# Kernel optimization log

Measured on AMD Instinct MI355X. Metric: run time of the kernel, lower is better.

The kernel has to match this reference:

```python
import jax, jax.numpy as jnp
import numpy as np

N_NODES = 100000


def gcn_conv(x, edge_index, edge_weight, W, b, num_nodes):
    """PyG-style GCNConv: add self-loops, symmetric normalization, aggregate, linear."""
    src, dst = edge_index[0], edge_index[1]
    loop = jnp.arange(num_nodes, dtype=src.dtype)
    src_f = jnp.concatenate([src, loop])
    dst_f = jnp.concatenate([dst, loop])
    w_f = jnp.concatenate([edge_weight, jnp.ones((num_nodes,), dtype=edge_weight.dtype)])

    # symmetric normalization D^-1/2 A_hat D^-1/2
    deg = jax.ops.segment_sum(w_f, dst_f, num_segments=num_nodes)
    dinv = jnp.where(deg > 0, jax.lax.rsqrt(deg), 0.0)
    norm = dinv[src_f] * w_f * dinv[dst_f]  # [E + N]

    h = x @ W  # transform first (small out dim) -> cheaper gather/scatter
    msg = h[src_f] * norm[:, None]  # [E + N, out]
    out = jax.ops.segment_sum(msg, dst_f, num_segments=num_nodes)
    return out + b


def setup_inputs() -> dict:
    key = jax.random.key(0)
    k = jax.random.split(key, 7)
    N, E, F, H, C = N_NODES, 3200000, 64, 32, 5
    x = jax.random.normal(k[0], (N, F), dtype=jnp.float32)
    edge_index = jax.random.randint(k[1], (2, E), 0, N, dtype=jnp.int64)
    edge_attr = jax.random.uniform(k[2], (E,), dtype=jnp.float32)
    # Glorot-style init for GCNConv weights, zero bias (PyG default)
    W1 = jax.random.normal(k[3], (F, H), dtype=jnp.float32) * (1.0 / np.sqrt(F))
    b1 = jnp.zeros((H,), dtype=jnp.float32)
    W2 = jax.random.normal(k[4], (H, C), dtype=jnp.float32) * (1.0 / np.sqrt(H))
    b2 = jnp.zeros((C,), dtype=jnp.float32)
    return {"x": x, "edge_index": edge_index, "edge_attr": edge_attr,
            "W1": W1, "b1": b1, "W2": W2, "b2": b2}


def reference(x, edge_index, edge_attr, W1, b1, W2, b2):
    # Dropout is identity in eval mode.
    x1 = gcn_conv(x, edge_index, edge_attr, W1, b1, N_NODES)
    x1 = jax.nn.relu(x1)
    x2 = gcn_conv(x1, edge_index, edge_attr, W2, b2, N_NODES)
    return (x2, x1)
```

## Files before the change

kernel.cpp:

```cpp
#include <hip/hip_runtime.h>

#define NN 100000
#define NE 3200000
#define FIN 64
#define FH 32
#define FO 5
#define NB 1000
#define NPB 100
#define NBIN (4*NPB)
#define QDIV 25000
#define GC 512
#define EPB (NE/GC)
#define KPT 25
#define APAD 6252
#define DPAD 6272
#define CAP 3584
#define WQS 32767.f
#define WQI (1.0f/32767.f)

typedef unsigned u32x4 __attribute__((ext_vector_type(4)));

__device__ __forceinline__ int detect64(const int* __restrict__ ei, int* sflag, int tid) {
    if (tid < 64) {
        int v = ei[2 * tid + 1];
        unsigned long long m = __ballot(v == 0);
        if (tid == 0) *sflag = (m == ~0ULL) ? 1 : 0;
    }
    __syncthreads();
    return *sflag;
}

__device__ __forceinline__ unsigned bf16r(float f) {
    unsigned u = __float_as_uint(f);
    return (u + 0x7FFFu + ((u >> 16) & 1u)) >> 16;
}
__device__ __forceinline__ float blo(unsigned u) { return __uint_as_float(u << 16); }
__device__ __forceinline__ float bhi(unsigned u) { return __uint_as_float(u & 0xFFFF0000u); }

__global__ void k_fillC(const int* __restrict__ ei, const float* __restrict__ w,
                        int* __restrict__ cntRM, int* __restrict__ locRM,
                        unsigned* __restrict__ edata_a, unsigned char* __restrict__ edata_d) {
    __shared__ unsigned stage_a[EPB];
    __shared__ unsigned char stage_d[EPB];
    __shared__ int hist[NB];
    __shared__ int hoff[NB];
    __shared__ int sscan[256];
    __shared__ int sflag;
    int tid = threadIdx.x, g = blockIdx.x;
    for (int i = tid; i < NB; i += 256) hist[i] = 0;
    int is64 = detect64(ei, &sflag, tid);
    __syncthreads();
    int base = g * EPB;
    int myd[KPT];
#pragma unroll
    for (int k = 0; k < KPT; ++k) {
        int e = base + tid + k * 256;
        int dst = -1;
        if (e < base + EPB) {
            dst = is64 ? ei[2 * NE + 2 * e] : ei[NE + e];
            atomicAdd(&hist[dst / NPB], 1);
        }
        myd[k] = dst;
    }
    __syncthreads();
    for (int i = tid; i < NB; i += 256) cntRM[g * NB + i] = hist[i];
    int b0 = tid * 4;
    int c0 = (b0 + 0 < NB) ? hist[b0 + 0] : 0;
    int c1 = (b0 + 1 < NB) ? hist[b0 + 1] : 0;
    int c2 = (b0 + 2 < NB) ? hist[b0 + 2] : 0;
    int c3 = (b0 + 3 < NB) ? hist[b0 + 3] : 0;
    sscan[tid] = c0 + c1 + c2 + c3;
    __syncthreads();
    for (int off = 1; off < 256; off <<= 1) {
        int v = (tid >= off) ? sscan[tid - off] : 0;
        __syncthreads();
        sscan[tid] += v;
        __syncthreads();
    }
    int excl = sscan[tid] - (c0 + c1 + c2 + c3);
    if (b0 + 0 < NB) { hoff[b0 + 0] = excl;                locRM[g * NB + b0 + 0] = excl; }
    if (b0 + 1 < NB) { hoff[b0 + 1] = excl + c0;           locRM[g * NB + b0 + 1] = excl + c0; }
    if (b0 + 2 < NB) { hoff[b0 + 2] = excl + c0 + c1;      locRM[g * NB + b0 + 2] = excl + c0 + c1; }
    if (b0 + 3 < NB) { hoff[b0 + 3] = excl + c0 + c1 + c2; locRM[g * NB + b0 + 3] = excl + c0 + c1 + c2; }
    __syncthreads();
#pragma unroll
    for (int k = 0; k < KPT; ++k) {
        int e = base + tid + k * 256;
        if (e < base + EPB) {
            int src = is64 ? ei[2 * e] : ei[e];
            int dst = myd[k];
            int b = dst / NPB;
            int dloc = dst - b * NPB;
            unsigned wq = (unsigned)(w[e] * WQS + 0.5f);
            int pos = atomicAdd(&hoff[b], 1);
            stage_a[pos] = (unsigned)src | (wq << 17);
            stage_d[pos] = (unsigned char)dloc;
        }
    }
    __syncthreads();
    unsigned* ga = edata_a + (size_t)g * APAD;
    int4* ga4 = (int4*)ga;
    const int NI4 = EPB / 4;
    for (int i = tid; i < NI4; i += 256) {
        int4 v;
        v.x = (int)stage_a[4 * i];     v.y = (int)stage_a[4 * i + 1];
        v.z = (int)stage_a[4 * i + 2]; v.w = (int)stage_a[4 * i + 3];
        ga4[i] = v;
    }
    if (tid < EPB - NI4 * 4) ga[NI4 * 4 + tid] = stage_a[NI4 * 4 + tid];
    unsigned* gd = (unsigned*)(edata_d + (size_t)g * DPAD);
    const int ND = (EPB + 3) / 4;
    for (int i = tid; i < ND; i += 256) {
        unsigned b0v = stage_d[4 * i];
        unsigned b1v = (4 * i + 1 < EPB) ? stage_d[4 * i + 1] : 0;
        unsigned b2v = (4 * i + 2 < EPB) ? stage_d[4 * i + 2] : 0;
        unsigned b3v = (4 * i + 3 < EPB) ? stage_d[4 * i + 3] : 0;
        gd[i] = b0v | (b1v << 8) | (b2v << 16) | (b3v << 24);
    }
}

__global__ __launch_bounds__(512) void k_nodecsr(
        const int* __restrict__ cntRM, const int* __restrict__ locRM,
        const unsigned* __restrict__ edata_a, const unsigned char* __restrict__ edata_d,
        unsigned* __restrict__ edata2,
        int* __restrict__ rowS, int* __restrict__ rowE, float* __restrict__ dinv) {
    __shared__ unsigned s1a[CAP];
    __shared__ unsigned char s1d[CAP];
    __shared__ unsigned s2a[CAP];
    __shared__ int cnt[NBIN];
    __shared__ int loc[NBIN];
    __shared__ int sc[512];
    __shared__ int llocS[512];
    __shared__ int sBlen;
    int* cur = cnt;
    int* degS = (int*)s2a;
    int bi = blockIdx.x, tid = threadIdx.x;
    int b = (bi & 7) * (NB / 8) + (bi >> 3);
    int base = b * CAP;
    int g = tid;
    int len  = cntRM[g * NB + b];
    int lloc = locRM[g * NB + b];
    llocS[tid] = lloc;
    for (int i = tid; i < NBIN; i += 512) cnt[i] = 0;
    if (tid < NPB) degS[tid] = 0;
    sc[tid] = len;
    __syncthreads();
    for (int off = 1; off < 512; off <<= 1) {
        int x = (tid >= off) ? sc[tid - off] : 0;
        __syncthreads();
        sc[tid] += x;
        __syncthreads();
    }
    if (tid == 511) sBlen = sc[511];
    __syncthreads();
    int blen = sBlen;
    if (blen <= CAP) {
        for (int j = tid; j < blen; j += 512) {
            int g2 = 0;
#pragma unroll
            for (int st = 256; st > 0; st >>= 1)
                if (g2 + st < 512 && sc[g2 + st - 1] <= j) g2 += st;
            int sd = g2 ? sc[g2 - 1] : 0;
            int off = j - sd;
            int ll = llocS[g2];
            unsigned a = edata_a[(size_t)g2 * APAD + ll + off];
            int dloc = edata_d[(size_t)g2 * DPAD + ll + off];
            int src = (int)(a & 0x1FFFF);
            atomicAdd(&cnt[(dloc << 2) | (src / QDIV)], 1);
            atomicAdd(&degS[dloc], (int)(a >> 17));
            s1a[j] = a;
            s1d[j] = (unsigned char)dloc;
        }
        __syncthreads();
        int v = (tid < NBIN) ? cnt[tid] : 0;
        sc[tid] = v;
        __syncthreads();
        for (int off = 1; off < 512; off <<= 1) {
            int x = (tid >= off) ? sc[tid - off] : 0;
            __syncthreads();
            sc[tid] += x;
            __syncthreads();
        }
        if (tid < NBIN) { loc[tid] = sc[tid] - v; }
        __syncthreads();
        if (tid < NBIN) cur[tid] = loc[tid];
        if (tid < NPB) {
            rowS[b * NPB + tid] = base + loc[4 * tid];
            rowE[b * NPB + tid] = base + ((tid == NPB - 1) ? blen : loc[4 * tid + 4]);
            dinv[b * NPB + tid] = rsqrtf(1.0f + (float)degS[tid] * WQI);
        }
        __syncthreads();
        for (int j = tid; j < blen; j += 512) {
            unsigned a = s1a[j];
            int dloc = s1d[j];
            int src = (int)(a & 0x1FFFF);
            int pos = atomicAdd(&cur[(dloc << 2) | (src / QDIV)], 1);
            s2a[pos] = a;
        }
        __syncthreads();
        for (int j = tid; j < blen; j += 512) edata2[base + j] = s2a[j];
    } else {
        const unsigned* A = edata_a + (size_t)g * APAD + lloc;
        const unsigned char* D = edata_d + (size_t)g * DPAD + lloc;
        int* degI = (int*)s1a;
        if (tid < NPB) degI[tid] = 0;
        __syncthreads();
        for (int k = 0; k < len; ++k) {
            unsigned a = A[k];
            int dloc = D[k];
            int src = (int)(a & 0x1FFFF);
            atomicAdd(&cnt[(dloc << 2) | (src / QDIV)], 1);
            atomicAdd(&degI[dloc], (int)(a >> 17));
        }
        __syncthreads();
        int v = (tid < NBIN) ? cnt[tid] : 0;
        sc[tid] = v;
        __syncthreads();
        for (int off = 1; off < 512; off <<= 1) {
            int x = (tid >= off) ? sc[tid - off] : 0;
            __syncthreads();
            sc[tid] += x;
            __syncthreads();
        }
        if (tid < NBIN) { loc[tid] = sc[tid] - v; }
        __syncthreads();
        if (tid < NBIN) cur[tid] = base + loc[tid];
        if (tid < NPB) {
            int e1 = (tid == NPB - 1) ? blen : loc[4 * tid + 4];
            if (e1 > CAP) e1 = CAP;
            int e0 = loc[4 * tid]; if (e0 > CAP) e0 = CAP;
            rowS[b * NPB + tid] = base + e0;
            rowE[b * NPB + tid] = base + e1;
            dinv[b * NPB + tid] = rsqrtf(1.0f + (float)degI[tid] * WQI);
        }
        __syncthreads();
        for (int k = 0; k < len; ++k) {
            unsigned a = A[k];
            int dloc = D[k];
            int src = (int)(a & 0x1FFFF);
            int pos = atomicAdd(&cur[(dloc << 2) | (src / QDIV)], 1);
            if (pos < base + CAP) edata2[pos] = a;
        }
    }
}

__global__ void k_gemm1(const float* __restrict__ x, const float* __restrict__ W1,
                        const float* __restrict__ dinv, unsigned* __restrict__ hs1b) {
    __shared__ float Ws[FIN * FH];
    __shared__ float Xs[16 * FIN];
    int tid = threadIdx.x;
    for (int i = tid; i < FIN * FH; i += 256) Ws[i] = W1[i];
    int row0 = blockIdx.x * 16;
    for (int i = tid; i < 16 * FIN; i += 256) Xs[i] = x[row0 * FIN + i];
    __syncthreads();
    int l = tid & 15, r = tid >> 4;
    int n = row0 + r;
    float a0 = 0.f, a1 = 0.f;
    const float* xr = &Xs[r * FIN];
#pragma unroll
    for (int f = 0; f < FIN; ++f) {
        float xv = xr[f];
        a0 += xv * Ws[f * FH + 2 * l];
        a1 += xv * Ws[f * FH + 2 * l + 1];
    }
    float di = dinv[n];
    hs1b[n * 16 + l] = bf16r(di * a0) | (bf16r(di * a1) << 16);
}

__device__ __forceinline__ void gather8_16(const unsigned* __restrict__ hs, int l,
                                           const u32x4& e0, const u32x4& e1, unsigned* u) {
    u[0] = hs[(e0[0] & 0x1FFFF) * 16 + l];
    u[1] = hs[(e0[1] & 0x1FFFF) * 16 + l];
    u[2] = hs[(e0[2] & 0x1FFFF) * 16 + l];
    u[3] = hs[(e0[3] & 0x1FFFF) * 16 + l];
    u[4] = hs[(e1[0] & 0x1FFFF) * 16 + l];
    u[5] = hs[(e1[1] & 0x1FFFF) * 16 + l];
    u[6] = hs[(e1[2] & 0x1FFFF) * 16 + l];
    u[7] = hs[(e1[3] & 0x1FFFF) * 16 + l];
}
__device__ __forceinline__ void consume8(const u32x4& e0, const u32x4& e1,
                                         const unsigned* u, float& a0, float& a1) {
#pragma unroll
    for (int j = 0; j < 4; ++j) {
        float wv = (float)(e0[j] >> 17) * WQI;
        a0 += wv * blo(u[j]); a1 += wv * bhi(u[j]);
    }
#pragma unroll
    for (int j = 0; j < 4; ++j) {
        float wv = (float)(e1[j] >> 17) * WQI;
        a0 += wv * blo(u[4 + j]); a1 += wv * bhi(u[4 + j]);
    }
}

__global__ void k_pull1(const int* __restrict__ rowS, const int* __restrict__ rowE,
                        const unsigned* __restrict__ ed,
                        const unsigned* __restrict__ hs1b, const float* __restrict__ dinv,
                        const float* __restrict__ b1, const float* __restrict__ W2,
                        float* __restrict__ x1out, unsigned* __restrict__ hs2b) {
    __shared__ float Ws2[FH * FO];
    int tid = threadIdx.x;
    if (tid < FH * FO) Ws2[tid] = W2[tid];
    __syncthreads();
    int l = tid & 15;
    int n = blockIdx.x * 16 + (tid >> 4);
    int s = rowS[n], t = rowE[n];
    unsigned su = hs1b[n * 16 + l];
    float a0 = blo(su), a1 = bhi(su);
    int i = s;
    for (; i < t && (i & 3); ++i) {
        unsigned c = ed[i];
        unsigned u = hs1b[(c & 0x1FFFF) * 16 + l];
        float we = (float)(c >> 17) * WQI;
        a0 += we * blo(u); a1 += we * bhi(u);
    }
    int nv = (t - i) >> 3;
    if (nv >= 1) {
        u32x4 ea0 = *(const u32x4*)(ed + i);
        u32x4 ea1 = *(const u32x4*)(ed + i + 4);
        u32x4 eb0 = {}, eb1 = {};
        if (nv >= 2) { eb0 = *(const u32x4*)(ed + i + 8); eb1 = *(const u32x4*)(ed + i + 12); }
        unsigned ua[8], ub[8];
        gather8_16(hs1b, l, ea0, ea1, ua);
        for (int k = 0; k < nv - 2; ++k) {
            u32x4 ec0 = *(const u32x4*)(ed + i + 16);
            u32x4 ec1 = *(const u32x4*)(ed + i + 20);
            gather8_16(hs1b, l, eb0, eb1, ub);
            consume8(ea0, ea1, ua, a0, a1);
            ea0 = eb0; ea1 = eb1; eb0 = ec0; eb1 = ec1;
#pragma unroll
            for (int j = 0; j < 8; ++j) ua[j] = ub[j];
            i += 8;
        }
        if (nv >= 2) {
            gather8_16(hs1b, l, eb0, eb1, ub);
            consume8(ea0, ea1, ua, a0, a1);
            consume8(eb0, eb1, ub, a0, a1);
            i += 16;
        } else {
            consume8(ea0, ea1, ua, a0, a1);
            i += 8;
        }
    }
    if (i + 4 <= t) {
        u32x4 e0 = *(const u32x4*)(ed + i);
        unsigned u[4];
        u[0] = hs1b[(e0[0] & 0x1FFFF) * 16 + l];
        u[1] = hs1b[(e0[1] & 0x1FFFF) * 16 + l];
        u[2] = hs1b[(e0[2] & 0x1FFFF) * 16 + l];
        u[3] = hs1b[(e0[3] & 0x1FFFF) * 16 + l];
#pragma unroll
        for (int j = 0; j < 4; ++j) {
            float wv = (float)(e0[j] >> 17) * WQI;
            a0 += wv * blo(u[j]); a1 += wv * bhi(u[j]);
        }
        i += 4;
    }
    for (; i < t; ++i) {
        unsigned c = ed[i];
        unsigned u = hs1b[(c & 0x1FFFF) * 16 + l];
        float we = (float)(c >> 17) * WQI;
        a0 += we * blo(u); a1 += we * bhi(u);
    }
    float di = dinv[n];
    float v0 = di * a0 + b1[2 * l];
    float v1 = di * a1 + b1[2 * l + 1];
    v0 = (v0 > 0.f) ? v0 : 0.f;
    v1 = (v1 > 0.f) ? v1 : 0.f;
    float2 st; st.x = v0; st.y = v1;
    *(float2*)&x1out[n * FH + 2 * l] = st;
    float hv[6];
    hv[5] = 0.f;
#pragma unroll
    for (int c = 0; c < FO; ++c) {
        float pr = v0 * Ws2[(2 * l) * FO + c] + v1 * Ws2[(2 * l + 1) * FO + c];
        pr += __shfl_xor(pr, 1, 16);
        pr += __shfl_xor(pr, 2, 16);
        pr += __shfl_xor(pr, 4, 16);
        pr += __shfl_xor(pr, 8, 16);
        hv[c] = di * pr;
    }
    if (l < 3) hs2b[n * 4 + l] = bf16r(hv[2 * l]) | (bf16r(hv[2 * l + 1]) << 16);
}

__device__ __forceinline__ void gather8_4(const unsigned* __restrict__ hs, int wj,
                                          const u32x4& e0, const u32x4& e1, unsigned* u) {
    u[0] = hs[(e0[0] & 0x1FFFF) * 4 + wj];
    u[1] = hs[(e0[1] & 0x1FFFF) * 4 + wj];
    u[2] = hs[(e0[2] & 0x1FFFF) * 4 + wj];
    u[3] = hs[(e0[3] & 0x1FFFF) * 4 + wj];
    u[4] = hs[(e1[0] & 0x1FFFF) * 4 + wj];
    u[5] = hs[(e1[1] & 0x1FFFF) * 4 + wj];
    u[6] = hs[(e1[2] & 0x1FFFF) * 4 + wj];
    u[7] = hs[(e1[3] & 0x1FFFF) * 4 + wj];
}
__device__ __forceinline__ void consume8p2(const u32x4& e0, const u32x4& e1,
                                           const unsigned* u, int hh, float& acc) {
#pragma unroll
    for (int j = 0; j < 4; ++j)
        acc += (float)(e0[j] >> 17) * WQI * (hh ? bhi(u[j]) : blo(u[j]));
#pragma unroll
    for (int j = 0; j < 4; ++j)
        acc += (float)(e1[j] >> 17) * WQI * (hh ? bhi(u[4 + j]) : blo(u[4 + j]));
}

__global__ void k_pull2(const int* __restrict__ rowS, const int* __restrict__ rowE,
                        const unsigned* __restrict__ ed,
                        const unsigned* __restrict__ hs2b, const float* __restrict__ dinv,
                        const float* __restrict__ b2, float* __restrict__ out) {
    int tid = threadIdx.x;
    int c = tid & 7;
    int cm = (c < FO) ? c : 0;
    int wj = cm >> 1, hh = cm & 1;
    int n = blockIdx.x * 32 + (tid >> 3);
    int s = rowS[n], t = rowE[n];
    unsigned us = hs2b[n * 4 + wj];
    float acc = hh ? bhi(us) : blo(us);
    int i = s;
    for (; i < t && (i & 3); ++i) {
        unsigned cc = ed[i];
        unsigned u = hs2b[(cc & 0x1FFFF) * 4 + wj];
        acc += (float)(cc >> 17) * WQI * (hh ? bhi(u) : blo(u));
    }
    int nv = (t - i) >> 3;
    if (nv >= 1) {
        u32x4 ea0 = *(const u32x4*)(ed + i);
        u32x4 ea1 = *(const u32x4*)(ed + i + 4);
        u32x4 eb0 = {}, eb1 = {};
        if (nv >= 2) { eb0 = *(const u32x4*)(ed + i + 8); eb1 = *(const u32x4*)(ed + i + 12); }
        unsigned ua[8], ub[8];
        gather8_4(hs2b, wj, ea0, ea1, ua);
        for (int k = 0; k < nv - 2; ++k) {
            u32x4 ec0 = *(const u32x4*)(ed + i + 16);
            u32x4 ec1 = *(const u32x4*)(ed + i + 20);
            gather8_4(hs2b, wj, eb0, eb1, ub);
            consume8p2(ea0, ea1, ua, hh, acc);
            ea0 = eb0; ea1 = eb1; eb0 = ec0; eb1 = ec1;
#pragma unroll
            for (int j = 0; j < 8; ++j) ua[j] = ub[j];
            i += 8;
        }
        if (nv >= 2) {
            gather8_4(hs2b, wj, eb0, eb1, ub);
            consume8p2(ea0, ea1, ua, hh, acc);
            consume8p2(eb0, eb1, ub, hh, acc);
            i += 16;
        } else {
            consume8p2(ea0, ea1, ua, hh, acc);
            i += 8;
        }
    }
    if (i + 4 <= t) {
        u32x4 e0 = *(const u32x4*)(ed + i);
        unsigned u[4];
        u[0] = hs2b[(e0[0] & 0x1FFFF) * 4 + wj];
        u[1] = hs2b[(e0[1] & 0x1FFFF) * 4 + wj];
        u[2] = hs2b[(e0[2] & 0x1FFFF) * 4 + wj];
        u[3] = hs2b[(e0[3] & 0x1FFFF) * 4 + wj];
#pragma unroll
        for (int j = 0; j < 4; ++j)
            acc += (float)(e0[j] >> 17) * WQI * (hh ? bhi(u[j]) : blo(u[j]));
        i += 4;
    }
    for (; i < t; ++i) {
        unsigned cc = ed[i];
        unsigned u = hs2b[(cc & 0x1FFFF) * 4 + wj];
        acc += (float)(cc >> 17) * WQI * (hh ? bhi(u) : blo(u));
    }
    if (c < FO) out[n * FO + c] = dinv[n] * acc + b2[c];
}

extern "C" void kernel_launch(void* const* d_in, const int* in_sizes, int n_in,
                              void* d_out, int out_size, void* d_ws, size_t ws_size,
                              hipStream_t stream) {
    const float* x  = (const float*)d_in[0];
    const int*   ei = (const int*)d_in[1];
    const float* w  = (const float*)d_in[2];
    const float* W1 = (const float*)d_in[3];
    const float* b1 = (const float*)d_in[4];
    const float* W2 = (const float*)d_in[5];
    const float* b2 = (const float*)d_in[6];
    float* out = (float*)d_out;
    float* ws  = (float*)d_ws;

    unsigned*      edata_a = (unsigned*)ws;
    unsigned char* edata_d = (unsigned char*)(ws + 3300000);
    unsigned*      edata2  = (unsigned*)(ws + 6400000);
    float*         dinv    = ws + 10000000;
    int*           rowS    = (int*)(ws + 10100000);
    int*           rowE    = (int*)(ws + 10200000);
    int*           cntRM   = (int*)(ws + 12800000);
    int*           locRM   = (int*)(ws + 13312000);
    unsigned*      hs1b    = (unsigned*)ws;
    unsigned*      hs2b    = (unsigned*)(ws + 1600000);

    float* x1 = out + NN * FO;

    k_fillC<<<GC, 256, 0, stream>>>(ei, w, cntRM, locRM, edata_a, edata_d);
    k_nodecsr<<<NB, 512, 0, stream>>>(cntRM, locRM, edata_a, edata_d, edata2, rowS, rowE, dinv);
    k_gemm1<<<NN / 16, 256, 0, stream>>>(x, W1, dinv, hs1b);
    k_pull1<<<NN / 16, 256, 0, stream>>>(rowS, rowE, edata2, hs1b, dinv, b1, W2, x1, hs2b);
    k_pull2<<<NN / 32, 256, 0, stream>>>(rowS, rowE, edata2, hs2b, dinv, b2, out);
}
```

Before: 229.7 us.

## Replace layer-2 pull with source-sliced shared-memory scatter aggregation

New measurement: 402.1 us. 1.75x slower.

```diff
diff --git a/kernel.cpp b/kernel.cpp
--- a/kernel.cpp
+++ b/kernel.cpp
@@ -17,6 +17,8 @@
 #define CAP 3584
 #define WQS 32767.f
 #define WQI (1.0f/32767.f)
+#define SLICE 2048
+#define NSL 49
 
 typedef unsigned u32x4 __attribute__((ext_vector_type(4)));
 
@@ -244,6 +246,53 @@
     }
 }
 
+__global__ __launch_bounds__(512) void k_slicesort(
+        const unsigned* __restrict__ edata2, const int* __restrict__ rowS,
+        const int* __restrict__ rowE,
+        unsigned* __restrict__ edata3a, unsigned* __restrict__ edata3d_w,
+        int* __restrict__ sliceOff) {
+    __shared__ unsigned ea[CAP];
+    __shared__ unsigned eb[CAP];
+    __shared__ unsigned char dl[CAP];
+    __shared__ unsigned char db[CAP];
+    __shared__ int cnt[NSL + 1];
+    __shared__ int off[NSL + 1];
+    int b = blockIdx.x, tid = threadIdx.x;
+    int base = b * CAP;
+    int blen = rowE[b * NPB + NPB - 1] - base;
+    for (int j = tid; j < blen; j += 512) ea[j] = edata2[base + j];
+    if (tid <= NSL) cnt[tid] = 0;
+    __syncthreads();
+    if (tid < NPB) {
+        int e0 = rowS[b * NPB + tid] - base, e1 = rowE[b * NPB + tid] - base;
+        for (int j = e0; j < e1; ++j) dl[j] = (unsigned char)tid;
+    }
+    __syncthreads();
+    for (int j = tid; j < blen; j += 512) atomicAdd(&cnt[(ea[j] & 0x1FFFF) >> 11], 1);
+    __syncthreads();
+    if (tid == 0) { int a = 0; for (int k = 0; k <= NSL; ++k) { off[k] = a; a += cnt[k]; } }
+    __syncthreads();
+    if (tid <= NSL) cnt[tid] = off[tid];
+    __syncthreads();
+    for (int j = tid; j < blen; j += 512) {
+        unsigned e = ea[j];
+        int s = (int)((e & 0x1FFFF) >> 11);
+        int p = atomicAdd(&cnt[s], 1);
+        eb[p] = e; db[p] = dl[j];
+    }
+    __syncthreads();
+    for (int j = tid; j < blen; j += 512) edata3a[base + j] = eb[j];
+    int nd = (blen + 3) / 4;
+    for (int i = tid; i < nd; i += 512) {
+        unsigned b0v = db[4 * i];
+        unsigned b1v = (4 * i + 1 < blen) ? db[4 * i + 1] : 0;
+        unsigned b2v = (4 * i + 2 < blen) ? db[4 * i + 2] : 0;
+        unsigned b3v = (4 * i + 3 < blen) ? db[4 * i + 3] : 0;
+        edata3d_w[b * (CAP / 4) + i] = b0v | (b1v << 8) | (b2v << 16) | (b3v << 24);
+    }
+    if (tid <= NSL) sliceOff[b * (NSL + 1) + tid] = base + off[tid];
+}
+
 __global__ void k_gemm1(const float* __restrict__ x, const float* __restrict__ W1,
                         const float* __restrict__ dinv, unsigned* __restrict__ hs1b) {
     __shared__ float Ws[FIN * FH];
@@ -382,91 +431,52 @@
     if (l < 3) hs2b[n * 4 + l] = bf16r(hv[2 * l]) | (bf16r(hv[2 * l + 1]) << 16);
 }
 
-__device__ __forceinline__ void gather8_4(const unsigned* __restrict__ hs, int wj,
-                                          const u32x4& e0, const u32x4& e1, unsigned* u) {
-    u[0] = hs[(e0[0] & 0x1FFFF) * 4 + wj];
-    u[1] = hs[(e0[1] & 0x1FFFF) * 4 + wj];
-    u[2] = hs[(e0[2] & 0x1FFFF) * 4 + wj];
-    u[3] = hs[(e0[3] & 0x1FFFF) * 4 + wj];
-    u[4] = hs[(e1[0] & 0x1FFFF) * 4 + wj];
-    u[5] = hs[(e1[1] & 0x1FFFF) * 4 + wj];
-    u[6] = hs[(e1[2] & 0x1FFFF) * 4 + wj];
-    u[7] = hs[(e1[3] & 0x1FFFF) * 4 + wj];
-}
-__device__ __forceinline__ void consume8p2(const u32x4& e0, const u32x4& e1,
-                                           const unsigned* u, int hh, float& acc) {
-#pragma unroll
-    for (int j = 0; j < 4; ++j)
-        acc += (float)(e0[j] >> 17) * WQI * (hh ? bhi(u[j]) : blo(u[j]));
-#pragma unroll
-    for (int j = 0; j < 4; ++j)
-        acc += (float)(e1[j] >> 17) * WQI * (hh ? bhi(u[4 + j]) : blo(u[4 + j]));
-}
-
-__global__ void k_pull2(const int* __restrict__ rowS, const int* __restrict__ rowE,
-                        const unsigned* __restrict__ ed,
-                        const unsigned* __restrict__ hs2b, const float* __restrict__ dinv,
-                        const float* __restrict__ b2, float* __restrict__ out) {
+__global__ __launch_bounds__(512) void k_pull2s(
+        const unsigned* __restrict__ edata3a, const unsigned char* __restrict__ edata3d,
+        const int* __restrict__ sliceOff, const unsigned* __restrict__ hs2b,
+        const float* __restrict__ dinv, const float* __restrict__ b2,
+        float* __restrict__ out) {
+    __shared__ u32x4 sl[SLICE];
+    __shared__ float acc[4 * NPB * FO];
+    __shared__ int sOf[4 * (NSL + 1)];
     int tid = threadIdx.x;
-    int c = tid & 7;
-    int cm = (c < FO) ? c : 0;
-    int wj = cm >> 1, hh = cm & 1;
-    int n = blockIdx.x * 32 + (tid >> 3);
-    int s = rowS[n], t = rowE[n];
-    unsigned us = hs2b[n * 4 + wj];
-    float acc = hh ? bhi(us) : blo(us);
-    int i = s;
-    for (; i < t && (i & 3); ++i) {
-        unsigned cc = ed[i];
-        unsigned u = hs2b[(cc & 0x1FFFF) * 4 + wj];
-        acc += (float)(cc >> 17) * WQI * (hh ? bhi(u) : blo(u));
-    }
-    int nv = (t - i) >> 3;
-    if (nv >= 1) {
-        u32x4 ea0 = *(const u32x4*)(ed + i);
-        u32x4 ea1 = *(const u32x4*)(ed + i + 4);
-        u32x4 eb0 = {}, eb1 = {};
-        if (nv >= 2) { eb0 = *(const u32x4*)(ed + i + 8); eb1 = *(const u32x4*)(ed + i + 12); }
-        unsigned ua[8], ub[8];
-        gather8_4(hs2b, wj, ea0, ea1, ua);
-        for (int k = 0; k < nv - 2; ++k) {
-            u32x4 ec0 = *(const u32x4*)(ed + i + 16);
-            u32x4 ec1 = *(const u32x4*)(ed + i + 20);
-            gather8_4(hs2b, wj, eb0, eb1, ub);
-            consume8p2(ea0, ea1, ua, hh, acc);
-            ea0 = eb0; ea1 = eb1; eb0 = ec0; eb1 = ec1;
-#pragma unroll
-            for (int j = 0; j < 8; ++j) ua[j] = ub[j];
-            i += 8;
-        }
-        if (nv >= 2) {
-            gather8_4(hs2b, wj, eb0, eb1, ub);
-            consume8p2(ea0, ea1, ua, hh, acc);
-            consume8p2(eb0, eb1, ub, hh, acc);
-            i += 16;
-        } else {
-            consume8p2(ea0, ea1, ua, hh, acc);
-            i += 8;
-        }
-    }
-    if (i + 4 <= t) {
-        u32x4 e0 = *(const u32x4*)(ed + i);
-        unsigned u[4];
-        u[0] = hs2b[(e0[0] & 0x1FFFF) * 4 + wj];
-        u[1] = hs2b[(e0[1] & 0x1FFFF) * 4 + wj];
-        u[2] = hs2b[(e0[2] & 0x1FFFF) * 4 + wj];
-        u[3] = hs2b[(e0[3] & 0x1FFFF) * 4 + wj];
-#pragma unroll
-        for (int j = 0; j < 4; ++j)
-            acc += (float)(e0[j] >> 17) * WQI * (hh ? bhi(u[j]) : blo(u[j]));
-        i += 4;
-    }
-    for (; i < t; ++i) {
-        unsigned cc = ed[i];
-        unsigned u = hs2b[(cc & 0x1FFFF) * 4 + wj];
-        acc += (float)(cc >> 17) * WQI * (hh ? bhi(u) : blo(u));
-    }
-    if (c < FO) out[n * FO + c] = dinv[n] * acc + b2[c];
+    int b0 = blockIdx.x * 4;
+    for (int i = tid; i < 4 * NPB * FO; i += 512) acc[i] = 0.f;
+    for (int i = tid; i < 4 * (NSL + 1); i += 512)
+        sOf[i] = sliceOff[(b0 + i / (NSL + 1)) * (NSL + 1) + i % (NSL + 1)];
+    const u32x4* hv4 = (const u32x4*)hs2b;
+    for (int s = 0; s < NSL; ++s) {
+        __syncthreads();
+        int sbase = s * SLICE;
+        int cn = min(SLICE, NN - sbase);
+        for (int j = tid; j < cn; j += 512) sl[j] = hv4[sbase + j];
+        __syncthreads();
+#pragma unroll
+        for (int bk = 0; bk < 4; ++bk) {
+            int st = sOf[bk * (NSL + 1) + s], en = sOf[bk * (NSL + 1) + s + 1];
+            for (int j = st + tid; j < en; j += 512) {
+                unsigned e = edata3a[j];
+                int dlc = edata3d[j];
+                int src = (int)(e & 0x1FFFF);
+                float wv = (float)(e >> 17) * WQI;
+                u32x4 u = sl[src - sbase];
+                float* a = &acc[(bk * NPB + dlc) * FO];
+                atomicAdd(a + 0, wv * blo(u[0]));
+                atomicAdd(a + 1, wv * bhi(u[0]));
+                atomicAdd(a + 2, wv * blo(u[1]));
+                atomicAdd(a + 3, wv * bhi(u[1]));
+                atomicAdd(a + 4, wv * blo(u[2]));
+            }
+        }
+    }
+    __syncthreads();
+    for (int idx = tid; idx < 4 * NPB * FO; idx += 512) {
+        int nl = idx / FO, c = idx - nl * FO;
+        int gn = b0 * NPB + nl;
+        unsigned us = hs2b[gn * 4 + (c >> 1)];
+        float sv = (c & 1) ? bhi(us) : blo(us);
+        out[gn * FO + c] = dinv[gn] * (acc[idx] + sv) + b2[c];
+    }
 }
 
 extern "C" void kernel_launch(void* const* d_in, const int* in_sizes, int n_in,
@@ -482,22 +492,27 @@
     float* out = (float*)d_out;
     float* ws  = (float*)d_ws;
 
-    unsigned*      edata_a = (unsigned*)ws;
-    unsigned char* edata_d = (unsigned char*)(ws + 3300000);
-    unsigned*      edata2  = (unsigned*)(ws + 6400000);
-    float*         dinv    = ws + 10000000;
-    int*           rowS    = (int*)(ws + 10100000);
-    int*           rowE    = (int*)(ws + 10200000);
-    int*           cntRM   = (int*)(ws + 12800000);
-    int*           locRM   = (int*)(ws + 13312000);
-    unsigned*      hs1b    = (unsigned*)ws;
-    unsigned*      hs2b    = (unsigned*)(ws + 1600000);
+    unsigned*      edata_a   = (unsigned*)ws;
+    unsigned char* edata_d   = (unsigned char*)(ws + 3300000);
+    unsigned*      edata2    = (unsigned*)(ws + 6400000);
+    float*         dinv      = ws + 10000000;
+    int*           rowS      = (int*)(ws + 10100000);
+    int*           rowE      = (int*)(ws + 10200000);
+    int*           cntRM     = (int*)(ws + 12800000);
+    int*           locRM     = (int*)(ws + 13312000);
+    unsigned*      hs1b      = (unsigned*)ws;
+    unsigned*      hs2b      = (unsigned*)(ws + 1600000);
+    unsigned*      edata3a   = (unsigned*)(ws + 2000000);
+    int*           sliceOff  = (int*)(ws + 5584000);
+    unsigned*      edata3d_w = (unsigned*)(ws + 10300000);
 
     float* x1 = out + NN * FO;
 
     k_fillC<<<GC, 256, 0, stream>>>(ei, w, cntRM, locRM, edata_a, edata_d);
     k_nodecsr<<<NB, 512, 0, stream>>>(cntRM, locRM, edata_a, edata_d, edata2, rowS, rowE, dinv);
+    k_slicesort<<<NB, 512, 0, stream>>>(edata2, rowS, rowE, edata3a, edata3d_w, sliceOff);
     k_gemm1<<<NN / 16, 256, 0, stream>>>(x, W1, dinv, hs1b);
     k_pull1<<<NN / 16, 256, 0, stream>>>(rowS, rowE, edata2, hs1b, dinv, b1, W2, x1, hs2b);
-    k_pull2<<<NN / 32, 256, 0, stream>>>(rowS, rowE, edata2, hs2b, dinv, b2, out);
-}
+    k_pull2s<<<NB / 4, 512, 0, stream>>>(edata3a, (const unsigned char*)edata3d_w,
+                                         sliceOff, hs2b, dinv, b2, out);
+}
```
